# Performance work log

Measured on AMD Instinct MI355X. Metric: run time of the kernel, lower is better.

The kernel has to match this reference:

```python
import jax, jax.numpy as jnp
import numpy as np

B, N, D, H = 4, 2048, 512, 8
HD = D // H  # head_dim = 64
EPS = 1e-5


def setup_inputs() -> dict:
    key = jax.random.key(0)
    ks = jax.random.split(key, 12)
    x = jax.random.normal(ks[0], (B, N, D), dtype=jnp.float32)
    adj = jax.random.randint(ks[1], (B, N, N), 0, 2, dtype=jnp.int32)
    # self-loops so no softmax row is fully masked
    adj = jnp.maximum(adj, jnp.eye(N, dtype=jnp.int32)[None, :, :])
    s = 1.0 / np.sqrt(D)
    Wq = jax.random.uniform(ks[2], (D, D), jnp.float32, -s, s)
    bq = jnp.zeros((D,), jnp.float32)
    Wk = jax.random.uniform(ks[3], (D, D), jnp.float32, -s, s)
    bk = jnp.zeros((D,), jnp.float32)
    Wv = jax.random.uniform(ks[4], (D, D), jnp.float32, -s, s)
    bv = jnp.zeros((D,), jnp.float32)
    Wo = jax.random.uniform(ks[5], (D, D), jnp.float32, -s, s)
    bo = jnp.zeros((D,), jnp.float32)
    gamma = jnp.ones((D,), jnp.float32)
    beta = jnp.zeros((D,), jnp.float32)
    return {"x": x, "adj": adj, "Wq": Wq, "bq": bq, "Wk": Wk, "bk": bk,
            "Wv": Wv, "bv": bv, "Wo": Wo, "bo": bo, "gamma": gamma, "beta": beta}


def reference(x, adj, Wq, bq, Wk, bk, Wv, bv, Wo, bo, gamma, beta):
    b, n, d = x.shape
    scale = 1.0 / np.sqrt(HD).astype(np.float32)
    # QKV projections -> (b, n, H, HD)
    q = (x @ Wq + bq).reshape(b, n, H, HD)
    k = (x @ Wk + bk).reshape(b, n, H, HD)
    v = (x @ Wv + bv).reshape(b, n, H, HD)
    # scores: (b, H, n, n)
    scores = jnp.einsum('bnhd,bmhd->bhnm', q, k) * scale
    mask = (adj == 0)[:, None, :, :]  # (b, 1, n, n)
    scores = jnp.where(mask, jnp.float32(-jnp.inf), scores)
    attn = jax.nn.softmax(scores, axis=-1)
    h = jnp.einsum('bhnm,bmhd->bnhd', attn, v).reshape(b, n, d)
    h = h @ Wo + bo
    # residual + LayerNorm
    y = h + x
    mu = jnp.mean(y, axis=-1, keepdims=True)
    var = jnp.mean(jnp.square(y - mu), axis=-1, keepdims=True)
    return (y - mu) * jax.lax.rsqrt(var + EPS) * gamma + beta
```

## Files before the change

### kernel.cpp

```cpp
#include <hip/hip_runtime.h>
#include <hip/hip_bf16.h>

#define Bsz 4
#define Nn 2048
#define Dd 512
#define Hh 8
#define HDim 64
#define MTOT (Bsz * Nn)

typedef unsigned short ush;
typedef __bf16 bf16x8 __attribute__((ext_vector_type(8)));
typedef float f32x4 __attribute__((ext_vector_type(4)));

__device__ __forceinline__ ush f2bf(float f) {
    unsigned u = __builtin_bit_cast(unsigned, f);
    unsigned r = (u + 0x7fffu + ((u >> 16) & 1u)) >> 16;
    return (ush)r;
}
__device__ __forceinline__ unsigned cvtpk(float a, float b) {
    unsigned r;
    asm("v_cvt_pk_bf16_f32 %0, %1, %2" : "=v"(r) : "v"(a), "v"(b));
    return r;
}

#define GLOAD_LDS(g, l)                                                       \
    __builtin_amdgcn_global_load_lds(                                         \
        (const __attribute__((address_space(1))) unsigned int*)(g),           \
        (__attribute__((address_space(3))) unsigned int*)(l), 16, 0, 0)

__global__ __launch_bounds__(256) void convert_bf16(const float* __restrict__ src,
                                                    ush* __restrict__ dst, int n) {
    int i = (blockIdx.x * 256 + threadIdx.x) * 4;
    if (i < n) {
        float4 v = *reinterpret_cast<const float4*>(src + i);
        dst[i + 0] = f2bf(v.x);
        dst[i + 1] = f2bf(v.y);
        dst[i + 2] = f2bf(v.z);
        dst[i + 3] = f2bf(v.w);
    }
}

__global__ __launch_bounds__(256) void transpose_bf16(const float* __restrict__ src,
                                                      ush* __restrict__ dst) {
    __shared__ ush tile[64][72];
    const int k0 = blockIdx.x * 64, n0 = blockIdx.y * 64;
    const int t = threadIdx.x;
    const int r = t >> 2, c = (t & 3) * 16;
#pragma unroll
    for (int i = 0; i < 4; ++i) {
        float4 v = *reinterpret_cast<const float4*>(src + (size_t)(k0 + r) * Dd + n0 + c + i * 4);
        tile[r][c + i * 4 + 0] = f2bf(v.x);
        tile[r][c + i * 4 + 1] = f2bf(v.y);
        tile[r][c + i * 4 + 2] = f2bf(v.z);
        tile[r][c + i * 4 + 3] = f2bf(v.w);
    }
    __syncthreads();
    const int rn = t >> 2, kc = (t & 3) * 16;
    ush ov[16];
#pragma unroll
    for (int j = 0; j < 16; ++j) ov[j] = tile[kc + j][rn];
    *reinterpret_cast<uint4*>(dst + (size_t)(n0 + rn) * Dd + k0 + kc) =
        *reinterpret_cast<uint4*>(&ov[0]);
    *reinterpret_cast<uint4*>(dst + (size_t)(n0 + rn) * Dd + k0 + kc + 8) =
        *reinterpret_cast<uint4*>(&ov[8]);
}

__global__ __launch_bounds__(256) void adj_to_bits(const int* __restrict__ adj,
                                                   unsigned* __restrict__ bits) {
    int idx = blockIdx.x * 256 + threadIdx.x;
    const int* p = adj + (size_t)(idx >> 6) * Nn + (idx & 63) * 32;
    unsigned m = 0;
#pragma unroll
    for (int v4 = 0; v4 < 8; ++v4) {
        int4 v = *reinterpret_cast<const int4*>(p + v4 * 4);
        if (v.x) m |= 1u << (v4 * 4 + 0);
        if (v.y) m |= 1u << (v4 * 4 + 1);
        if (v.z) m |= 1u << (v4 * 4 + 2);
        if (v.w) m |= 1u << (v4 * 4 + 3);
    }
    bits[idx] = m;
}

__global__ __launch_bounds__(256) void gemm128(const ush* __restrict__ A,
                                               const ush* __restrict__ Wt,
                                               const float* __restrict__ bq,
                                               const float* __restrict__ bk,
                                               const float* __restrict__ bv,
                                               ush* __restrict__ outQ,
                                               ush* __restrict__ outK,
                                               ush* __restrict__ outVt,
                                               float* __restrict__ outF, int fused) {
    __shared__ __align__(16) ush As[2][128][32];
    __shared__ __align__(16) ush Bs[2][128][32];
    const int t = threadIdx.x, lane = t & 63, w = t >> 6;
    const int ln = lane & 15, gr = lane >> 4;
    const int m0 = blockIdx.x * 128, n0 = blockIdx.y * 128;
    const int wm = w >> 1, wn = w & 1;

    f32x4 acc[4][4] = {};
    const int srow = lane >> 2, schk = (lane & 3) * 8;

#define STG(buf, k0)                                                               \
    {                                                                              \
        _Pragma("unroll") for (int o = 0; o < 2; ++o) {                            \
            int r0 = o * 64 + w * 16;                                              \
            int rr = r0 + srow;                                                    \
            GLOAD_LDS(A + (size_t)(m0 + rr) * Dd + (k0) + schk, &As[buf][r0][0]);  \
            GLOAD_LDS(Wt + (size_t)(n0 + rr) * Dd + (k0) + schk, &Bs[buf][r0][0]); \
        }                                                                          \
    }

    STG(0, 0);
    __syncthreads();

    for (int it = 0; it < 16; ++it) {
        const int buf = it & 1;
        if (it < 15) STG(buf ^ 1, (it + 1) * 32);
        bf16x8 af[4], bf_[4];
#pragma unroll
        for (int i = 0; i < 4; ++i)
            af[i] = *reinterpret_cast<const bf16x8*>(&As[buf][wm * 64 + i * 16 + ln][gr * 8]);
#pragma unroll
        for (int j = 0; j < 4; ++j)
            bf_[j] = *reinterpret_cast<const bf16x8*>(&Bs[buf][wn * 64 + j * 16 + ln][gr * 8]);
#pragma unroll
        for (int i = 0; i < 4; ++i)
#pragma unroll
            for (int j = 0; j < 4; ++j)
                acc[i][j] = __builtin_amdgcn_mfma_f32_16x16x32_bf16(af[i], bf_[j], acc[i][j], 0, 0, 0);
        __syncthreads();
    }

    const float SCL = 0.125f * 1.44269504f;
    if (fused) {
        const int qkv = blockIdx.y >> 2;
        const float* bias = (qkv == 0) ? bq : ((qkv == 1) ? bk : bv);
        const float scale = (qkv == 0) ? SCL : 1.0f;
#pragma unroll
        for (int i = 0; i < 4; ++i) {
#pragma unroll
            for (int j = 0; j < 4; ++j) {
#pragma unroll
                for (int r = 0; r < 4; ++r) {
                    int row = m0 + wm * 64 + i * 16 + gr * 4 + r;
                    int colq = (n0 & 511) + wn * 64 + j * 16 + ln;
                    float v = (acc[i][j][r] + bias[colq]) * scale;
                    int b = row >> 11, n = row & (Nn - 1);
                    int h = colq >> 6, hd = colq & 63;
                    if (qkv == 2)
                        outVt[(((size_t)(b * Hh + h)) * HDim + hd) * Nn + n] = f2bf(v);
                    else {
                        ush* o = (qkv == 0) ? outQ : outK;
                        o[(((size_t)(b * Hh + h)) * Nn + n) * HDim + hd] = f2bf(v);
                    }
                }
            }
        }
    } else {
#pragma unroll
        for (int i = 0; i < 4; ++i) {
#pragma unroll
            for (int j = 0; j < 4; ++j) {
#pragma unroll
                for (int r = 0; r < 4; ++r) {
                    int row = m0 + wm * 64 + i * 16 + gr * 4 + r;
                    int col = n0 + wn * 64 + j * 16 + ln;
                    outF[(size_t)row * Dd + col] = acc[i][j][r] + bq[col];
                }
            }
        }
    }
#undef STG
}

__global__ __launch_bounds__(256) void attn_kernel(const ush* __restrict__ Q,
                                                   const ush* __restrict__ K,
                                                   const ush* __restrict__ Vt,
                                                   const unsigned* __restrict__ bits,
                                                   ush* __restrict__ O) {
    __shared__ __align__(16) ush Ktile[2][64][64];
    __shared__ __align__(16) ush Vtile[2][64][64];
    __shared__ __align__(16) ush Pl[4][16][64];
    const int t = threadIdx.x, lane = t & 63, w = t >> 6;
    const int ln = lane & 15, gr = lane >> 4;
    const int blk = blockIdx.x;
    const int qt = blk & 31;
    const int bh = blk >> 5;
    const int b = bh >> 3, h = bh & 7;
    const int q0 = qt * 64 + w * 16;

    const ush* Qb = Q + (size_t)bh * Nn * HDim;
    const ush* Kb = K + (size_t)bh * Nn * HDim;
    const ush* Vb = Vt + (size_t)bh * HDim * Nn;
    const unsigned* rowbits = bits + ((size_t)b * Nn + q0 + ln) * (Nn / 32);

    char* plbase = (char*)&Pl[w][0][0];
    const int lnm = ln & 7;

    const int srow_in_op = lane >> 3;
    const int schk = lane & 7;

#define STAGE_K(buf, kv0)                                                              \
    {                                                                                  \
        _Pragma("unroll") for (int o = 0; o < 2; ++o) {                                \
            int r0 = o * 32 + w * 8;                                                   \
            int rr = r0 + srow_in_op;                                                  \
            int cc = schk ^ (rr & 7);                                                  \
            GLOAD_LDS(Kb + (size_t)((kv0) + rr) * HDim + cc * 8, &Ktile[buf][r0][0]);  \
        }                                                                              \
    }
#define STAGE_V(buf, kv0)                                                              \
    {                                                                                  \
        _Pragma("unroll") for (int o = 0; o < 2; ++o) {                                \
            int r0 = o * 32 + w * 8;                                                   \
            int rr = r0 + srow_in_op;                                                  \
            int cc = schk ^ (rr & 7);                                                  \
            GLOAD_LDS(Vb + (size_t)rr * Nn + (kv0) + cc * 8, &Vtile[buf][r0][0]);      \
        }                                                                              \
    }

    bf16x8 bq0 = *reinterpret_cast<const bf16x8*>(Qb + (size_t)(q0 + ln) * HDim + gr * 8);
    bf16x8 bq1 = *reinterpret_cast<const bf16x8*>(Qb + (size_t)(q0 + ln) * HDim + 32 + gr * 8);

    f32x4 accO[4] = {};
    float mrow = -1e30f, lrow = 0.f;

    STAGE_K(0, 0);
    STAGE_V(0, 0);
    __syncthreads();

    for (int step = 0; step < 32; ++step) {
        const int kv0 = step * 64;
        const int buf = step & 1;
        if (step < 31) {
            STAGE_K(buf ^ 1, kv0 + 64);
            STAGE_V(buf ^ 1, kv0 + 64);
        }

        unsigned w0 = rowbits[kv0 >> 5];
        unsigned w1 = rowbits[(kv0 >> 5) + 1];

        f32x4 s[4];
#pragma unroll
        for (int kt = 0; kt < 4; ++kt) {
            bf16x8 a0 = *reinterpret_cast<const bf16x8*>(
                &Ktile[buf][kt * 16 + ln][((gr) ^ lnm) * 8]);
            bf16x8 a1 = *reinterpret_cast<const bf16x8*>(
                &Ktile[buf][kt * 16 + ln][((4 + gr) ^ lnm) * 8]);
            f32x4 z = {};
            z = __builtin_amdgcn_mfma_f32_16x16x32_bf16(a0, bq0, z, 0, 0, 0);
            s[kt] = __builtin_amdgcn_mfma_f32_16x16x32_bf16(a1, bq1, z, 0, 0, 0);
        }

        float p[4][4];
        float mk[4];
#pragma unroll
        for (int kt = 0; kt < 4; ++kt) {
            unsigned wsel = (kt >= 2) ? w1 : w0;
#pragma unroll
            for (int r = 0; r < 4; ++r) {
                float sv = s[kt][r];
                int bit = (kt * 16 + 4 * gr + r) & 31;
                p[kt][r] = ((wsel >> bit) & 1u) ? sv : -1e30f;
            }
            mk[kt] = fmaxf(fmaxf(p[kt][0], p[kt][1]), fmaxf(p[kt][2], p[kt][3]));
        }
        float mc = fmaxf(fmaxf(mk[0], mk[1]), fmaxf(mk[2], mk[3]));
        mc = fmaxf(mc, __shfl_xor(mc, 16));
        mc = fmaxf(mc, __shfl_xor(mc, 32));

        if (!__all(mc - mrow <= 8.0f)) {
            float mn = fmaxf(mrow, mc);
            float alpha = __builtin_amdgcn_exp2f(mrow - mn);
            mrow = mn;
            lrow *= alpha;
#pragma unroll
            for (int t2 = 0; t2 < 4; ++t2)
#pragma unroll
                for (int r = 0; r < 4; ++r) accO[t2][r] *= alpha;
        }

        float sk[4];
#pragma unroll
        for (int kt = 0; kt < 4; ++kt) {
#pragma unroll
            for (int r = 0; r < 4; ++r) p[kt][r] = __builtin_amdgcn_exp2f(p[kt][r] - mrow);
            sk[kt] = (p[kt][0] + p[kt][1]) + (p[kt][2] + p[kt][3]);
        }
        float ps = (sk[0] + sk[1]) + (sk[2] + sk[3]);
        ps += __shfl_xor(ps, 16);
        ps += __shfl_xor(ps, 32);
        lrow += ps;

#pragma unroll
        for (int kt = 0; kt < 4; ++kt) {
            unsigned pk0 = cvtpk(p[kt][0], p[kt][1]);
            unsigned pk1 = cvtpk(p[kt][2], p[kt][3]);
            int blkw = (2 * kt + (gr >> 1)) ^ lnm;
            *reinterpret_cast<uint2*>(plbase + ln * 128 + blkw * 16 + 8 * (gr & 1)) =
                make_uint2(pk0, pk1);
        }
#pragma unroll
        for (int c = 0; c < 2; ++c) {
            bf16x8 pf = *reinterpret_cast<const bf16x8*>(
                plbase + ln * 128 + (((4 * c + gr) ^ lnm) * 16));
#pragma unroll
            for (int t2 = 0; t2 < 4; ++t2) {
                bf16x8 vf = *reinterpret_cast<const bf16x8*>(
                    &Vtile[buf][t2 * 16 + ln][((c * 4 + gr) ^ lnm) * 8]);
                accO[t2] = __builtin_amdgcn_mfma_f32_16x16x32_bf16(vf, pf, accO[t2], 0, 0, 0);
            }
        }
        __syncthreads();
    }

    float inv = 1.0f / lrow;
#pragma unroll
    for (int t2 = 0; t2 < 4; ++t2) {
        unsigned o0 = cvtpk(accO[t2][0] * inv, accO[t2][1] * inv);
        unsigned o1 = cvtpk(accO[t2][2] * inv, accO[t2][3] * inv);
        int blkw = (2 * t2 + (gr >> 1)) ^ lnm;
        *reinterpret_cast<uint2*>(plbase + ln * 128 + blkw * 16 + 8 * (gr & 1)) =
            make_uint2(o0, o1);
    }
    int qr = lane >> 2, cs = lane & 3;
#pragma unroll
    for (int half = 0; half < 2; ++half) {
        int blkr = (cs * 2 + half) ^ (qr & 7);
        uint4 val = *reinterpret_cast<const uint4*>(plbase + qr * 128 + blkr * 16);
        *reinterpret_cast<uint4*>(O + ((size_t)(b * Nn + qt * 64 + w * 16 + qr)) * Dd +
                                  h * 64 + cs * 16 + half * 8) = val;
    }
#undef STAGE_K
#undef STAGE_V
}

__global__ __launch_bounds__(256) void ln_kernel(const float* __restrict__ hbuf,
                                                 const float* __restrict__ x,
                                                 const float* __restrict__ gamma,
                                                 const float* __restrict__ beta,
                                                 float* __restrict__ out) {
    const int row = blockIdx.x;
    const int t = threadIdx.x;
    const float* hr = hbuf + (size_t)row * Dd;
    const float* xr = x + (size_t)row * Dd;
    float y0 = hr[t] + xr[t];
    float y1 = hr[t + 256] + xr[t + 256];

    __shared__ float red[4];
    float s = y0 + y1;
#pragma unroll
    for (int m = 32; m; m >>= 1) s += __shfl_xor(s, m);
    if ((t & 63) == 0) red[t >> 6] = s;
    __syncthreads();
    float mu = (red[0] + red[1] + red[2] + red[3]) * (1.0f / Dd);

    float d0 = y0 - mu, d1 = y1 - mu;
    float vs = d0 * d0 + d1 * d1;
#pragma unroll
    for (int m = 32; m; m >>= 1) vs += __shfl_xor(vs, m);
    __syncthreads();
    if ((t & 63) == 0) red[t >> 6] = vs;
    __syncthreads();
    float var = (red[0] + red[1] + red[2] + red[3]) * (1.0f / Dd);
    float rs = rsqrtf(var + 1e-5f);

    out[(size_t)row * Dd + t] = d0 * rs * gamma[t] + beta[t];
    out[(size_t)row * Dd + t + 256] = d1 * rs * gamma[t + 256] + beta[t + 256];
}

extern "C" void kernel_launch(void* const* d_in, const int* in_sizes, int n_in,
                              void* d_out, int out_size, void* d_ws, size_t ws_size,
                              hipStream_t stream) {
    const float* x = (const float*)d_in[0];
    const int* adj = (const int*)d_in[1];
    const float* Wq = (const float*)d_in[2];
    const float* bq = (const float*)d_in[3];
    const float* Wk = (const float*)d_in[4];
    const float* bk = (const float*)d_in[5];
    const float* Wv = (const float*)d_in[6];
    const float* bv = (const float*)d_in[7];
    const float* Wo = (const float*)d_in[8];
    const float* bo = (const float*)d_in[9];
    const float* gamma = (const float*)d_in[10];
    const float* beta = (const float*)d_in[11];
    float* out = (float*)d_out;

    const size_t MD = (size_t)MTOT * Dd;
    const size_t WW = (size_t)Dd * Dd;
    ush* ws = (ush*)d_ws;
    ush* xb = ws;
    ush* Wqkvb = xb + MD;
    ush* Wob = Wqkvb + 3 * WW;
    ush* Qb = Wob + WW;
    ush* Kb = Qb + MD;
    ush* Vtb = Kb + MD;
    ush* Ob = Vtb + MD;
    float* hbuf = (float*)(Ob + MD);
    unsigned* bitsbuf = (unsigned*)hbuf;

    convert_bf16<<<dim3((int)(MD / 1024)), dim3(256), 0, stream>>>(x, xb, (int)MD);
    dim3 tg(Dd / 64, Dd / 64), bb(256);
    transpose_bf16<<<tg, bb, 0, stream>>>(Wq, Wqkvb);
    transpose_bf16<<<tg, bb, 0, stream>>>(Wk, Wqkvb + WW);
    transpose_bf16<<<tg, bb, 0, stream>>>(Wv, Wqkvb + 2 * WW);
    transpose_bf16<<<tg, bb, 0, stream>>>(Wo, Wob);

    adj_to_bits<<<dim3(MTOT * 64 / 256), dim3(256), 0, stream>>>(adj, bitsbuf);

    gemm128<<<dim3(MTOT / 128, 12), bb, 0, stream>>>(xb, Wqkvb, bq, bk, bv,
                                                     Qb, Kb, Vtb, nullptr, 1);

    attn_kernel<<<dim3(Bsz * Hh * (Nn / 64)), bb, 0, stream>>>(Qb, Kb, Vtb, bitsbuf, Ob);

    gemm128<<<dim3(MTOT / 128, 4), bb, 0, stream>>>(Ob, Wob, bo, nullptr, nullptr,
                                                    nullptr, nullptr, nullptr, hbuf, 0);

    ln_kernel<<<dim3(MTOT), bb, 0, stream>>>(hbuf, x, gamma, beta, out);
}
```

Baseline: 289.7 us.

## Swizzle GEMM LDS tiles, vectorize V-transpose stores, make softmax rescale unconditional

The GEMM staging now XOR-swizzles the 8-element k-chunks by row, so the MFMA fragment reads from LDS no longer bank-conflict. The fused QKV epilogue hoists the bias load, and for V it packs four consecutive tokens into one 8-byte store into the transposed layout instead of four scalar stores. In the attention kernel the lazy, threshold-gated online-softmax rescale is replaced by an unconditional rescale every tile. This removes a wave-wide vote and branch but adds 16 multiplies and an exp2 per tile.

```diff
diff --git a/kernel.cpp b/kernel.cpp
--- a/kernel.cpp
+++ b/kernel.cpp
@@ -98,20 +98,24 @@
     const int wm = w >> 1, wn = w & 1;
 
     f32x4 acc[4][4] = {};
-    const int srow = lane >> 2, schk = (lane & 3) * 8;
-
-#define STG(buf, k0)                                                               \
-    {                                                                              \
-        _Pragma("unroll") for (int o = 0; o < 2; ++o) {                            \
-            int r0 = o * 64 + w * 16;                                              \
-            int rr = r0 + srow;                                                    \
-            GLOAD_LDS(A + (size_t)(m0 + rr) * Dd + (k0) + schk, &As[buf][r0][0]);  \
-            GLOAD_LDS(Wt + (size_t)(n0 + rr) * Dd + (k0) + schk, &Bs[buf][r0][0]); \
-        }                                                                          \
+    const int srow = lane >> 2;
+    const int cpos = lane & 3;
+
+#define STG(buf, k0)                                                              \
+    {                                                                             \
+        _Pragma("unroll") for (int o = 0; o < 2; ++o) {                           \
+            int r0 = o * 64 + w * 16;                                             \
+            int rr = r0 + srow;                                                   \
+            int ck = (cpos ^ (rr & 3)) * 8;                                       \
+            GLOAD_LDS(A + (size_t)(m0 + rr) * Dd + (k0) + ck, &As[buf][r0][0]);   \
+            GLOAD_LDS(Wt + (size_t)(n0 + rr) * Dd + (k0) + ck, &Bs[buf][r0][0]);  \
+        }                                                                         \
     }
 
     STG(0, 0);
     __syncthreads();
+
+    const int fchk = (gr ^ (ln & 3)) * 8;
 
     for (int it = 0; it < 16; ++it) {
         const int buf = it & 1;
@@ -119,10 +123,10 @@
         bf16x8 af[4], bf_[4];
 #pragma unroll
         for (int i = 0; i < 4; ++i)
-            af[i] = *reinterpret_cast<const bf16x8*>(&As[buf][wm * 64 + i * 16 + ln][gr * 8]);
+            af[i] = *reinterpret_cast<const bf16x8*>(&As[buf][wm * 64 + i * 16 + ln][fchk]);
 #pragma unroll
         for (int j = 0; j < 4; ++j)
-            bf_[j] = *reinterpret_cast<const bf16x8*>(&Bs[buf][wn * 64 + j * 16 + ln][gr * 8]);
+            bf_[j] = *reinterpret_cast<const bf16x8*>(&Bs[buf][wn * 64 + j * 16 + ln][fchk]);
 #pragma unroll
         for (int i = 0; i < 4; ++i)
 #pragma unroll
@@ -140,18 +144,25 @@
         for (int i = 0; i < 4; ++i) {
 #pragma unroll
             for (int j = 0; j < 4; ++j) {
-#pragma unroll
-                for (int r = 0; r < 4; ++r) {
-                    int row = m0 + wm * 64 + i * 16 + gr * 4 + r;
-                    int colq = (n0 & 511) + wn * 64 + j * 16 + ln;
-                    float v = (acc[i][j][r] + bias[colq]) * scale;
-                    int b = row >> 11, n = row & (Nn - 1);
-                    int h = colq >> 6, hd = colq & 63;
-                    if (qkv == 2)
-                        outVt[(((size_t)(b * Hh + h)) * HDim + hd) * Nn + n] = f2bf(v);
-                    else {
-                        ush* o = (qkv == 0) ? outQ : outK;
-                        o[(((size_t)(b * Hh + h)) * Nn + n) * HDim + hd] = f2bf(v);
+                int colq = (n0 & 511) + wn * 64 + j * 16 + ln;
+                int h = colq >> 6, hd = colq & 63;
+                float bi = bias[colq];
+                if (qkv == 2) {
+                    int row0 = m0 + wm * 64 + i * 16 + gr * 4;
+                    int b = row0 >> 11, nidx = row0 & (Nn - 1);
+                    unsigned p0 = cvtpk(acc[i][j][0] + bi, acc[i][j][1] + bi);
+                    unsigned p1 = cvtpk(acc[i][j][2] + bi, acc[i][j][3] + bi);
+                    *reinterpret_cast<uint2*>(
+                        outVt + (((size_t)(b * Hh + h)) * HDim + hd) * Nn + nidx) =
+                        make_uint2(p0, p1);
+                } else {
+                    ush* o = (qkv == 0) ? outQ : outK;
+#pragma unroll
+                    for (int r = 0; r < 4; ++r) {
+                        int row = m0 + wm * 64 + i * 16 + gr * 4 + r;
+                        int b = row >> 11, nidx = row & (Nn - 1);
+                        float v = (acc[i][j][r] + bi) * scale;
+                        o[(((size_t)(b * Hh + h)) * Nn + nidx) * HDim + hd] = f2bf(v);
                     }
                 }
             }
@@ -161,11 +172,12 @@
         for (int i = 0; i < 4; ++i) {
 #pragma unroll
             for (int j = 0; j < 4; ++j) {
+                int col = n0 + wn * 64 + j * 16 + ln;
+                float bi = bq[col];
 #pragma unroll
                 for (int r = 0; r < 4; ++r) {
                     int row = m0 + wm * 64 + i * 16 + gr * 4 + r;
-                    int col = n0 + wn * 64 + j * 16 + ln;
-                    outF[(size_t)row * Dd + col] = acc[i][j][r] + bq[col];
+                    outF[(size_t)row * Dd + col] = acc[i][j][r] + bi;
                 }
             }
         }
@@ -268,29 +280,25 @@
         float mc = fmaxf(fmaxf(mk[0], mk[1]), fmaxf(mk[2], mk[3]));
         mc = fmaxf(mc, __shfl_xor(mc, 16));
         mc = fmaxf(mc, __shfl_xor(mc, 32));
-
-        if (!__all(mc - mrow <= 8.0f)) {
-            float mn = fmaxf(mrow, mc);
-            float alpha = __builtin_amdgcn_exp2f(mrow - mn);
-            mrow = mn;
-            lrow *= alpha;
-#pragma unroll
-            for (int t2 = 0; t2 < 4; ++t2)
-#pragma unroll
-                for (int r = 0; r < 4; ++r) accO[t2][r] *= alpha;
-        }
+        float mn = fmaxf(mrow, mc);
+        float alpha = __builtin_amdgcn_exp2f(mrow - mn);
+        mrow = mn;
 
         float sk[4];
 #pragma unroll
         for (int kt = 0; kt < 4; ++kt) {
 #pragma unroll
-            for (int r = 0; r < 4; ++r) p[kt][r] = __builtin_amdgcn_exp2f(p[kt][r] - mrow);
+            for (int r = 0; r < 4; ++r) p[kt][r] = __builtin_amdgcn_exp2f(p[kt][r] - mn);
             sk[kt] = (p[kt][0] + p[kt][1]) + (p[kt][2] + p[kt][3]);
         }
         float ps = (sk[0] + sk[1]) + (sk[2] + sk[3]);
         ps += __shfl_xor(ps, 16);
         ps += __shfl_xor(ps, 32);
-        lrow += ps;
+        lrow = lrow * alpha + ps;
+#pragma unroll
+        for (int t2 = 0; t2 < 4; ++t2)
+#pragma unroll
+            for (int r = 0; r < 4; ++r) accO[t2][r] *= alpha;
 
 #pragma unroll
         for (int kt = 0; kt < 4; ++kt) {
```

Measured after the change: 265.6 us. 8.3% less time.
